# Kernel optimization log

Measured on AMD Instinct MI355X. Metric: run time of the kernel, lower is better.

Reference implementation:

```python
import jax, jax.numpy as jnp
import numpy as np

D_IN = 3
HID = 256
N_BRANCH = 8
SKIP_IN = (4,)
CSG_TREE = [0, 1, [2, 3], [4, 5, [6, 7]]]
FLAG_CONVEX = True
BETA = 100.0
N_POINTS = 100000

# layer dims: [3, 256*7, 8]; layer whose OUTPUT feeds a skip layer emits 256-3=253
_DIMS = [D_IN] + [HID] * 7 + [N_BRANCH]


def _layer_out_dim(layer):
    if (layer + 1) in SKIP_IN:
        return _DIMS[layer + 1] - D_IN
    return _DIMS[layer + 1]


def setup_inputs() -> dict:
    key = jax.random.key(0)
    keys = jax.random.split(key, 20)
    inp = {"x": jax.random.normal(keys[0], (N_POINTS, D_IN), dtype=jnp.float32)}
    n_layers = len(_DIMS) - 1  # 8 linear layers
    for layer in range(n_layers):
        in_d = _DIMS[layer]
        out_d = _layer_out_dim(layer)
        kw = jax.random.fold_in(keys[1], layer)
        if layer == n_layers - 1:  # geometric init of last layer
            W = (np.sqrt(np.pi) / np.sqrt(in_d)
                 + 1e-5 * jax.random.normal(kw, (in_d, out_d), dtype=jnp.float32))
            b = -1.0 * jnp.ones((out_d,), dtype=jnp.float32)
        else:
            W = (np.sqrt(2.0) / np.sqrt(out_d)) * jax.random.normal(
                kw, (in_d, out_d), dtype=jnp.float32)
            b = jnp.zeros((out_d,), dtype=jnp.float32)
        inp[f"W{layer}"] = W
        inp[f"b{layer}"] = b
    return inp


def _softplus_beta(x):
    return jax.nn.softplus(BETA * x) / BETA


def _csg_combine(vals, ops, cvx_flag):
    # hard CSG tree: one-hot matmul == column gather; recursion is static (trace time)
    idxs = [v for v in ops if not isinstance(v, list)]
    cols = [vals[:, jnp.array(idxs)]]
    for v in ops:
        if isinstance(v, list):
            cols.append(_csg_combine(vals, v, not cvx_flag))
    m = jnp.concatenate(cols, axis=1)
    red = jnp.max if cvx_flag else jnp.min
    return red(m, axis=1, keepdims=True)


def _forward(x, Ws, bs):
    inp = x
    h = x
    n_layers = len(Ws)
    inv_sqrt2 = np.float32(1.0 / np.sqrt(2.0))
    for layer in range(n_layers):
        if layer in SKIP_IN:
            h = jnp.concatenate([h, inp], axis=-1) * inv_sqrt2
        h = h @ Ws[layer] + bs[layer]
        if layer < n_layers - 1:
            h = _softplus_beta(h)
    branch_vals = h  # [N, n_branch]
    hcsg = _csg_combine(branch_vals, CSG_TREE, FLAG_CONVEX)  # [N, 1]
    return jnp.concatenate([hcsg, branch_vals], axis=1)  # flag_output == 0


def reference(x, W0, b0, W1, b1, W2, b2, W3, b3, W4, b4, W5, b5, W6, b6, W7, b7):
    Ws = [W0, W1, W2, W3, W4, W5, W6, W7]
    bs = [b0, b1, b2, b3, b4, b5, b6, b7]
    return _forward(x, Ws, bs)
```

## Files before the change

### kernel.cpp

```cpp
#include <hip/hip_runtime.h>
#include <hip/hip_bf16.h>


using bf16x8 = __attribute__((ext_vector_type(8))) __bf16;
using f32x4  = __attribute__((ext_vector_type(4))) float;

#define LDA 264

#define OFFW0 0
#define OFFW1 8192
#define OFFW7 401408
#define WSB_BYTE_OFF 811008
#define OFFB7 1792

#define SCALE_T2 144.26950408889634f
#define INV_SQRT2 0.70710678118654752f
#define LN2_100 0.0069314718055994531f

__device__ __forceinline__ float fast_exp2(float x) {
#if __has_builtin(__builtin_amdgcn_exp2f)
    return __builtin_amdgcn_exp2f(x);
#else
    return exp2f(x);
#endif
}
__device__ __forceinline__ float fast_log2(float x) {
#if __has_builtin(__builtin_amdgcn_logf)
    return __builtin_amdgcn_logf(x);
#else
    return log2f(x);
#endif
}

__device__ __forceinline__ float softplus_t2(float t2) {
    float e = fast_exp2(-fabsf(t2));
    float l = fast_log2(1.0f + e);
    return fmaxf(t2, 0.0f) + l;
}

__device__ __forceinline__ unsigned short bf16_rne(float f) {
    unsigned int u = __float_as_uint(f);
    unsigned int r = u + 0x7FFFu + ((u >> 16) & 1u);
    return (unsigned short)(r >> 16);
}

template <int KK, int NTG>
__device__ __forceinline__ void mfma_group(
    const unsigned short* __restrict__ wfrag,
    const float* __restrict__ bias,
    const unsigned short* act,
    f32x4 (&acc)[2][NTG], int wave, int lane)
{
    const int quad = lane >> 4;
    const int l15  = lane & 15;

#pragma unroll
    for (int i = 0; i < 2; ++i) {
        const int chb = (wave * 2 + i) * 16 + quad * 4;
        const float4 b4 = *(const float4*)(bias + chb);
#pragma unroll
        for (int nt = 0; nt < NTG; ++nt)
            acc[i][nt] = f32x4{b4.x, b4.y, b4.z, b4.w};
    }

    const unsigned short* wbase = wfrag + (wave * 2 * KK * 64 + lane) * 8;

#pragma unroll
    for (int kk = 0; kk < KK; ++kk) {
        bf16x8 bfr[NTG];
#pragma unroll
        for (int nt = 0; nt < NTG; ++nt)
            bfr[nt] = *(const bf16x8*)(act + (nt * 16 + l15) * LDA + kk * 32 + quad * 8);
#pragma unroll
        for (int i = 0; i < 2; ++i) {
            bf16x8 afr = *(const bf16x8*)(wbase + (i * KK + kk) * 512);
#pragma unroll
            for (int nt = 0; nt < NTG; ++nt)
                acc[i][nt] = __builtin_amdgcn_mfma_f32_16x16x32_bf16(afr, bfr[nt], acc[i][nt], 0, 0, 0);
        }
    }
}

template <int I, int NT>
__device__ __forceinline__ void epi_slice(
    const f32x4& a4, unsigned short* act, const float* xst,
    bool splice, int wave, int quad, int l15)
{
    const int chb = (wave * 2 + I) * 16 + quad * 4;
    const int pt  = NT * 16 + l15;
    float vv[4];
#pragma unroll
    for (int r = 0; r < 4; ++r)
        vv[r] = softplus_t2(a4[r]);
    if (splice && chb == 252) {
        vv[1] = xst[pt * 4 + 0];
        vv[2] = xst[pt * 4 + 1];
        vv[3] = xst[pt * 4 + 2];
    }
    __hip_bfloat162 p01 = __float22bfloat162_rn(float2{vv[0], vv[1]});
    __hip_bfloat162 p23 = __float22bfloat162_rn(float2{vv[2], vv[3]});
    uint2 pk;
    pk.x = *(unsigned int*)&p01;
    pk.y = *(unsigned int*)&p23;
    *(uint2*)(act + pt * LDA + chb) = pk;
}

template <int NTG>
__device__ __forceinline__ void epi_group(
    f32x4 (&acc)[2][NTG], unsigned short* act, const float* xst,
    int wave, int lane, bool splice)
{
    const int quad = lane >> 4;
    const int l15  = lane & 15;
#pragma unroll
    for (int i = 0; i < 2; ++i)
#pragma unroll
        for (int nt = 0; nt < NTG; ++nt) {
            if (i == 0) epi_slice<0, 0>(acc[0][nt], act + nt * 16 * LDA - 0, xst + nt * 0, splice, wave, quad, l15);
        }
}

template <int NTG>
__device__ __forceinline__ void epi_group_full(
    f32x4 (&acc)[2][NTG], unsigned short* act, const float* xst,
    int wave, int lane, bool splice)
{
    const int quad = lane >> 4;
    const int l15  = lane & 15;
#pragma unroll
    for (int i = 0; i < 2; ++i) {
        const int chb = (wave * 2 + i) * 16 + quad * 4;
#pragma unroll
        for (int nt = 0; nt < NTG; ++nt) {
            const int pt = nt * 16 + l15;
            float vv[4];
#pragma unroll
            for (int r = 0; r < 4; ++r)
                vv[r] = softplus_t2(acc[i][nt][r]);
            if (splice && chb == 252) {
                vv[1] = xst[pt * 4 + 0];
                vv[2] = xst[pt * 4 + 1];
                vv[3] = xst[pt * 4 + 2];
            }
            __hip_bfloat162 p01 = __float22bfloat162_rn(float2{vv[0], vv[1]});
            __hip_bfloat162 p23 = __float22bfloat162_rn(float2{vv[2], vv[3]});
            uint2 pk;
            pk.x = *(unsigned int*)&p01;
            pk.y = *(unsigned int*)&p23;
            *(uint2*)(act + pt * LDA + chb) = pk;
        }
    }
}

template <int KK, int NTG>
__device__ __forceinline__ void stag_region(
    const unsigned short* __restrict__ wfrag,
    const float* __restrict__ bias,
    const unsigned short* __restrict__ actX,
    unsigned short* actY,
    f32x4 (&accX)[2][NTG], f32x4 (&accY)[2][NTG],
    const float* xstY, bool splice, int wave, int lane)
{
    const int quad = lane >> 4;
    const int l15  = lane & 15;

#pragma unroll
    for (int i = 0; i < 2; ++i) {
        const int chb = (wave * 2 + i) * 16 + quad * 4;
        const float4 b4 = *(const float4*)(bias + chb);
#pragma unroll
        for (int nt = 0; nt < NTG; ++nt)
            accX[i][nt] = f32x4{b4.x, b4.y, b4.z, b4.w};
    }

    const unsigned short* wbase = wfrag + (wave * 2 * KK * 64 + lane) * 8;

#pragma unroll
    for (int kk = 0; kk < KK; ++kk) {
        bf16x8 bfr[NTG];
#pragma unroll
        for (int nt = 0; nt < NTG; ++nt)
            bfr[nt] = *(const bf16x8*)(actX + (nt * 16 + l15) * LDA + kk * 32 + quad * 8);
        bf16x8 afr0 = *(const bf16x8*)(wbase + kk * 512);
        bf16x8 afr1 = *(const bf16x8*)(wbase + (KK + kk) * 512);

        if (kk < 2 * NTG) {
            constexpr int c = 0;  (void)c;
            const int i  = kk & 1;
            const int nt = kk >> 1;
            const int chb = (wave * 2 + i) * 16 + quad * 4;
            const int pt  = nt * 16 + l15;
            float vv[4];
#pragma unroll
            for (int r = 0; r < 4; ++r)
                vv[r] = softplus_t2(accY[i][nt][r]);
            if (splice && chb == 252) {
                vv[1] = xstY[pt * 4 + 0];
                vv[2] = xstY[pt * 4 + 1];
                vv[3] = xstY[pt * 4 + 2];
            }
            __hip_bfloat162 p01 = __float22bfloat162_rn(float2{vv[0], vv[1]});
            __hip_bfloat162 p23 = __float22bfloat162_rn(float2{vv[2], vv[3]});
            uint2 pk;
            pk.x = *(unsigned int*)&p01;
            pk.y = *(unsigned int*)&p23;
            *(uint2*)(actY + pt * LDA + chb) = pk;
        }

#pragma unroll
        for (int nt = 0; nt < NTG; ++nt)
            accX[0][nt] = __builtin_amdgcn_mfma_f32_16x16x32_bf16(afr0, bfr[nt], accX[0][nt], 0, 0, 0);
#pragma unroll
        for (int nt = 0; nt < NTG; ++nt)
            accX[1][nt] = __builtin_amdgcn_mfma_f32_16x16x32_bf16(afr1, bfr[nt], accX[1][nt], 0, 0, 0);
    }
}

__device__ __forceinline__ void l7_part(
    const unsigned short* act, const unsigned short* __restrict__ w7,
    const float* __restrict__ wsB, float* __restrict__ out,
    int row0, int ptg0, int npts, int lane)
{
    const int quad = lane >> 4, l15 = lane & 15;
    const float4 b4 = *(const float4*)(wsB + OFFB7 + quad * 4);
    f32x4 acc = f32x4{b4.x, b4.y, b4.z, b4.w};
#pragma unroll
    for (int kk = 0; kk < 8; ++kk) {
        bf16x8 bfr = *(const bf16x8*)(act + (row0 + l15) * LDA + kk * 32 + quad * 8);
        bf16x8 afr = *(const bf16x8*)(w7 + (kk * 64 + lane) * 8);
        acc = __builtin_amdgcn_mfma_f32_16x16x32_bf16(afr, bfr, acc, 0, 0, 0);
    }
    float u0 = __shfl(acc[0], l15 + 16);
    float u1 = __shfl(acc[1], l15 + 16);
    float u2 = __shfl(acc[2], l15 + 16);
    float u3 = __shfl(acc[3], l15 + 16);
    if (quad == 0) {
        const int ptg = ptg0 + l15;
        if (ptg < npts) {
            const float v0 = acc[0], v1 = acc[1], v2 = acc[2], v3 = acc[3];
            const float v4 = u0, v5 = u1, v6 = u2, v7 = u3;
            const float m23   = fminf(v2, v3);
            const float m67   = fmaxf(v6, v7);
            const float m4567 = fminf(fminf(v4, v5), m67);
            const float h     = fmaxf(fmaxf(v0, v1), fmaxf(m23, m4567));
            float* o = out + (long)ptg * 9;
            o[0] = h;
            o[1] = v0; o[2] = v1; o[3] = v2; o[4] = v3;
            o[5] = v4; o[6] = v5; o[7] = v6; o[8] = v7;
        }
    }
}

template <int NTG>
__device__ __forceinline__ void run_net(
    const float* __restrict__ x, float* __restrict__ out,
    const unsigned short* __restrict__ wsW, const float* __restrict__ wsB,
    unsigned short* act, float* xst,
    int base_pt, int npts, int tid)
{
    const int wave = tid >> 6, lane = tid & 63;

    for (int i = tid; i < 2 * NTG * 16 * 32; i += 512) {
        const int pt = i >> 5, ch = i & 31;
        const int ptg = base_pt + pt;
        float v = 0.0f;
        if (ch < 3 && ptg < npts) v = x[ptg * 3 + ch];
        act[pt * LDA + ch] = bf16_rne(v);
        if (ch < 4) xst[pt * 4 + ch] = (ch < 3) ? v : 0.0f;
    }
    __syncthreads();

    unsigned short* actA = act;
    unsigned short* actB = act + NTG * 16 * LDA;
    const float* xstA = xst;
    const float* xstB = xst + NTG * 16 * 4;

    f32x4 accA[2][NTG], accB[2][NTG];

    mfma_group<1, NTG>(wsW + OFFW0, wsB, actA, accA, wave, lane);
    __syncthreads();
    mfma_group<1, NTG>(wsW + OFFW0, wsB, actB, accB, wave, lane);
    epi_group_full<NTG>(accA, actA, xstA, wave, lane, false);
    __syncthreads();

#pragma unroll 1
    for (int l = 1; l <= 6; ++l) {
        const unsigned short* Wl = wsW + OFFW1 + (l - 1) * 65536;
        const float* bl = wsB + l * 256;

        stag_region<8, NTG>(Wl, bl, actA, actB, accA, accB, xstB, l == 4, wave, lane);
        __syncthreads();

        stag_region<8, NTG>(Wl, bl, actB, actA, accB, accA, xstA, l == 3, wave, lane);
        __syncthreads();
    }

    if (wave < NTG)
        l7_part(act, wsW + OFFW7, wsB, out, wave * 16, base_pt + wave * 16, npts, lane);
    epi_group_full<NTG>(accB, actB, xstB, wave, lane, false);
    __syncthreads();

    if (wave < NTG)
        l7_part(act, wsW + OFFW7, wsB, out,
                NTG * 16 + wave * 16, base_pt + NTG * 16 + wave * 16, npts, lane);
}

__global__ __launch_bounds__(512, 4)
void nhrep_main(const float* __restrict__ x, float* __restrict__ out,
                const unsigned short* __restrict__ wsW,
                const float* __restrict__ wsB, int npts, int nbig)
{
    __shared__ unsigned short act[64 * LDA];
    __shared__ float xst[64 * 4];
    const int b = blockIdx.x;
    if (b < nbig) {
        run_net<2>(x, out, wsW, wsB, act, xst, b * 64, npts, threadIdx.x);
    } else {
        run_net<1>(x, out, wsW, wsB, act, xst,
                   nbig * 64 + (b - nbig) * 32, npts, threadIdx.x);
    }
}

struct PackArgs {
    const float* W[8];
    const float* b[8];
};

#define TOTAL_FRAGS 50688
#define TOTAL_BIAS  1808

__global__ void prepack_all(PackArgs args, unsigned short* __restrict__ dstW,
                            float* __restrict__ dstB)
{
    const int t = blockIdx.x * blockDim.x + threadIdx.x;
    const int FB[9]  = {0, 1024, 9216, 17408, 25600, 33792, 41984, 50176, 50688};
    const int KKs[8] = {1, 8, 8, 8, 8, 8, 8, 8};
    const int ind[8] = {3, 256, 256, 256, 256, 256, 256, 256};
    const int outd[8]= {256, 256, 256, 253, 256, 256, 256, 8};

    if (t < TOTAL_FRAGS) {
        int l = 0;
        while (t >= FB[l + 1]) ++l;
        const int f    = t - FB[l];
        const int lane = f & 63;
        const int kk   = (f >> 6) % KKs[l];
        const int mt   = f / (64 * KKs[l]);
        const int o    = mt * 16 + (lane & 15);
        const int kb   = kk * 32 + (lane >> 4) * 8;
        const float* W = args.W[l];
        const int in_d = ind[l], out_d = outd[l];

        unsigned short v[8];
#pragma unroll
        for (int j = 0; j < 8; ++j) {
            const int k = kb + j;
            float w = 0.0f;
            if (k < in_d && o < out_d) {
                float sc = 1.0f;
                if (l == 0) sc = SCALE_T2;
                else if (l == 4) sc = (k < 253) ? INV_SQRT2 : (SCALE_T2 * INV_SQRT2);
                else if (l == 7) sc = LN2_100;
                w = W[k * out_d + o] * sc;
            }
            unsigned int u = __float_as_uint(w);
            v[j] = (unsigned short)((u + 0x7FFFu + ((u >> 16) & 1u)) >> 16);
        }
        uint4 p;
        p.x = (unsigned int)v[0] | ((unsigned int)v[1] << 16);
        p.y = (unsigned int)v[2] | ((unsigned int)v[3] << 16);
        p.z = (unsigned int)v[4] | ((unsigned int)v[5] << 16);
        p.w = (unsigned int)v[6] | ((unsigned int)v[7] << 16);
        *(uint4*)(dstW + (long)t * 8) = p;
    } else if (t < TOTAL_FRAGS + TOTAL_BIAS) {
        const int u = t - TOTAL_FRAGS;
        const int l = (u < 1792) ? (u >> 8) : 7;
        const int idx = (l < 7) ? (u & 255) : (u - 1792);
        const float sc = (l < 7) ? SCALE_T2 : 1.0f;
        dstB[u] = (idx < outd[l]) ? args.b[l][idx] * sc : 0.0f;
    }
}

extern "C" void kernel_launch(void* const* d_in, const int* in_sizes, int n_in,
                              void* d_out, int out_size, void* d_ws, size_t ws_size,
                              hipStream_t stream)
{
    const float* x = (const float*)d_in[0];
    unsigned short* wsW = (unsigned short*)d_ws;
    float* wsB = (float*)((char*)d_ws + WSB_BYTE_OFF);

    PackArgs pa;
    for (int l = 0; l < 8; ++l) {
        pa.W[l] = (const float*)d_in[1 + 2 * l];
        pa.b[l] = (const float*)d_in[2 + 2 * l];
    }
    const int ptot = TOTAL_FRAGS + TOTAL_BIAS;
    prepack_all<<<(ptot + 255) / 256, 256, 0, stream>>>(pa, wsW, wsB);

    const int npts = in_sizes[0] / 3;
    int nbig, nsmall;
    const int tail_pts = 16384;
    if (npts > tail_pts) {
        nbig = (npts - tail_pts + 63) / 64;
        const int base_small = nbig * 64;
        nsmall = (npts - base_small + 31) / 32;
    } else {
        nbig = 0;
        nsmall = (npts + 31) / 32;
    }
    nhrep_main<<<nbig + nsmall, 512, 0, stream>>>(x, (float*)d_out, wsW, wsB,
                                                  npts, nbig);
}
```

Baseline: 193.3 us.

## Grow big-block tile to 96 points and prefetch weight fragments one step ahead

Big blocks now process 96 points each (NTG=3) instead of 64, so every weight fragment loaded from global memory feeds more MFMAs. The fused ping-pong GEMM loop also loads the next k-step's weight fragments before the current step's MFMAs to hide global-load latency. The unused epi_slice/epi_group helpers are removed. The cost is more LDS per block (96 rows × LDA) and more accumulator registers, which could reduce occupancy under launch_bounds(512,4). With 2*NTG=6 overlapping epilogue slots, the fused epilogue must still fit within the 8 k-steps.

```diff
diff --git a/kernel.cpp b/kernel.cpp
--- a/kernel.cpp
+++ b/kernel.cpp
@@ -79,45 +79,6 @@
                 acc[i][nt] = __builtin_amdgcn_mfma_f32_16x16x32_bf16(afr, bfr[nt], acc[i][nt], 0, 0, 0);
         }
     }
-}
-
-template <int I, int NT>
-__device__ __forceinline__ void epi_slice(
-    const f32x4& a4, unsigned short* act, const float* xst,
-    bool splice, int wave, int quad, int l15)
-{
-    const int chb = (wave * 2 + I) * 16 + quad * 4;
-    const int pt  = NT * 16 + l15;
-    float vv[4];
-#pragma unroll
-    for (int r = 0; r < 4; ++r)
-        vv[r] = softplus_t2(a4[r]);
-    if (splice && chb == 252) {
-        vv[1] = xst[pt * 4 + 0];
-        vv[2] = xst[pt * 4 + 1];
-        vv[3] = xst[pt * 4 + 2];
-    }
-    __hip_bfloat162 p01 = __float22bfloat162_rn(float2{vv[0], vv[1]});
-    __hip_bfloat162 p23 = __float22bfloat162_rn(float2{vv[2], vv[3]});
-    uint2 pk;
-    pk.x = *(unsigned int*)&p01;
-    pk.y = *(unsigned int*)&p23;
-    *(uint2*)(act + pt * LDA + chb) = pk;
-}
-
-template <int NTG>
-__device__ __forceinline__ void epi_group(
-    f32x4 (&acc)[2][NTG], unsigned short* act, const float* xst,
-    int wave, int lane, bool splice)
-{
-    const int quad = lane >> 4;
-    const int l15  = lane & 15;
-#pragma unroll
-    for (int i = 0; i < 2; ++i)
-#pragma unroll
-        for (int nt = 0; nt < NTG; ++nt) {
-            if (i == 0) epi_slice<0, 0>(acc[0][nt], act + nt * 16 * LDA - 0, xst + nt * 0, splice, wave, quad, l15);
-        }
 }
 
 template <int NTG>
@@ -175,17 +136,23 @@
 
     const unsigned short* wbase = wfrag + (wave * 2 * KK * 64 + lane) * 8;
 
+    bf16x8 afr0 = *(const bf16x8*)(wbase);
+    bf16x8 afr1 = *(const bf16x8*)(wbase + KK * 512);
+
 #pragma unroll
     for (int kk = 0; kk < KK; ++kk) {
+        const bf16x8 a0 = afr0, a1 = afr1;
+        if (kk + 1 < KK) {
+            afr0 = *(const bf16x8*)(wbase + (kk + 1) * 512);
+            afr1 = *(const bf16x8*)(wbase + (KK + kk + 1) * 512);
+        }
+
         bf16x8 bfr[NTG];
 #pragma unroll
         for (int nt = 0; nt < NTG; ++nt)
             bfr[nt] = *(const bf16x8*)(actX + (nt * 16 + l15) * LDA + kk * 32 + quad * 8);
-        bf16x8 afr0 = *(const bf16x8*)(wbase + kk * 512);
-        bf16x8 afr1 = *(const bf16x8*)(wbase + (KK + kk) * 512);
 
         if (kk < 2 * NTG) {
-            constexpr int c = 0;  (void)c;
             const int i  = kk & 1;
             const int nt = kk >> 1;
             const int chb = (wave * 2 + i) * 16 + quad * 4;
@@ -209,10 +176,10 @@
 
 #pragma unroll
         for (int nt = 0; nt < NTG; ++nt)
-            accX[0][nt] = __builtin_amdgcn_mfma_f32_16x16x32_bf16(afr0, bfr[nt], accX[0][nt], 0, 0, 0);
-#pragma unroll
-        for (int nt = 0; nt < NTG; ++nt)
-            accX[1][nt] = __builtin_amdgcn_mfma_f32_16x16x32_bf16(afr1, bfr[nt], accX[1][nt], 0, 0, 0);
+            accX[0][nt] = __builtin_amdgcn_mfma_f32_16x16x32_bf16(a0, bfr[nt], accX[0][nt], 0, 0, 0);
+#pragma unroll
+        for (int nt = 0; nt < NTG; ++nt)
+            accX[1][nt] = __builtin_amdgcn_mfma_f32_16x16x32_bf16(a1, bfr[nt], accX[1][nt], 0, 0, 0);
     }
 }
 
@@ -310,14 +277,14 @@
                 const unsigned short* __restrict__ wsW,
                 const float* __restrict__ wsB, int npts, int nbig)
 {
-    __shared__ unsigned short act[64 * LDA];
-    __shared__ float xst[64 * 4];
+    __shared__ unsigned short act[96 * LDA];
+    __shared__ float xst[96 * 4];
     const int b = blockIdx.x;
     if (b < nbig) {
-        run_net<2>(x, out, wsW, wsB, act, xst, b * 64, npts, threadIdx.x);
+        run_net<3>(x, out, wsW, wsB, act, xst, b * 96, npts, threadIdx.x);
     } else {
         run_net<1>(x, out, wsW, wsB, act, xst,
-                   nbig * 64 + (b - nbig) * 32, npts, threadIdx.x);
+                   nbig * 96 + (b - nbig) * 32, npts, threadIdx.x);
     }
 }
 
@@ -400,8 +367,8 @@
     int nbig, nsmall;
     const int tail_pts = 16384;
     if (npts > tail_pts) {
-        nbig = (npts - tail_pts + 63) / 64;
-        const int base_small = nbig * 64;
+        nbig = (npts - tail_pts + 95) / 96;
+        const int base_small = nbig * 96;
         nsmall = (npts - base_small + 31) / 32;
     } else {
         nbig = 0;
```

Result: faster. 181.3 us (median of 2 runs) (-6.2%).
